# Performance work log

Measured on AMD Instinct MI355X. Metric: run time of the kernel, lower is better.

Reference implementation:

```python
import jax, jax.numpy as jnp
import numpy as np

B, K, D, H, A = 8192, 10, 64, 128, 16
E = K * (K - 1)
# lexicographic ordered pairs (i,j), i != j -- matches adj.nonzero() and sorted(Dict.keys())
_PAIRS = np.array([(i, j) for i in range(K) for j in range(K) if i != j], dtype=np.int32)
SRC = jnp.asarray(_PAIRS[:, 0])  # message for edge (i,j) is aggregated at node i (row)
DST = jnp.asarray(_PAIRS[:, 1])


def setup_inputs() -> dict:
    key = jax.random.key(0)
    k1, k2, k3, k4, k5, k6 = jax.random.split(key, 6)
    F = D + H + A  # node MLP input dim
    return {
        "states": jax.random.normal(k1, (B, K, D), jnp.float32),
        "action_vec": jax.random.normal(k2, (B, K, A), jnp.float32),
        # one Linear(2D -> H) per ordered pair, stacked [E, 2D, H]
        "W_edge": jax.random.normal(k3, (E, 2 * D, H), jnp.float32) * (1.0 / np.sqrt(2 * D)),
        "b_edge": jax.random.normal(k4, (E, H), jnp.float32) * 0.01,
        # one Linear(D+H+A -> D) per node, stacked [K, F, D]
        "W_node": jax.random.normal(k5, (K, F, D), jnp.float32) * (1.0 / np.sqrt(F)),
        "b_node": jax.random.normal(k6, (K, D), jnp.float32) * 0.01,
    }


def reference(states, action_vec, W_edge, b_edge, W_node, b_node):
    # states: [B,K,D], action_vec: [B,K,A]
    b, k, d = states.shape
    # gather endpoints per ordered edge: [B,E,2D]
    pair_feat = jnp.concatenate([states[:, SRC, :], states[:, DST, :]], axis=-1)
    # per-edge-type Linear + tanh, batched as one grouped GEMM: [B,E,H]
    msg = jnp.tanh(jnp.einsum('bef,efh->beh', pair_feat, W_edge) + b_edge)
    # unsorted_segment_sum over source node index (row): [B,K,H]
    agg = jnp.zeros((b, k, msg.shape[-1]), msg.dtype).at[:, SRC, :].add(msg)
    # node input: [x, action, agg] -> per-node Linear + tanh: [B,K,D]
    node_in = jnp.concatenate([states, action_vec, agg], axis=-1)
    out = jnp.tanh(jnp.einsum('bkf,kfd->bkd', node_in, W_node) + b_node)
    return out
```

## Files before the change

kernel.cpp:

```cpp
#include <hip/hip_runtime.h>

typedef _Float16 f16;
typedef _Float16 f16x4 __attribute__((ext_vector_type(4)));
typedef _Float16 f16x8 __attribute__((ext_vector_type(8)));
typedef float    f32x4 __attribute__((ext_vector_type(4)));

#define S2C 2.88539008177792681472f

#define OFF_STF  0u
#define OFF_AC   5242880u
#define OFF_WEF  6553600u
#define OFF_WNF  8028160u
#define OFF_BE2  8171520u
#define OFF_Z    8195840u

__device__ __forceinline__ float fast_exp2(float x){
#if __has_builtin(__builtin_amdgcn_exp2f)
    return __builtin_amdgcn_exp2f(x);
#else
    return exp2f(x);
#endif
}
__device__ __forceinline__ float fast_rcp(float x){
#if __has_builtin(__builtin_amdgcn_rcpf)
    return __builtin_amdgcn_rcpf(x);
#else
    return 1.0f/x;
#endif
}

#define MFMA16(a,b,c) __builtin_amdgcn_mfma_f32_16x16x32_f16(a,b,c,0,0,0)

__global__ void prep(const float* __restrict__ st, const float* __restrict__ ac,
                     const float* __restrict__ We, const float* __restrict__ be,
                     const float* __restrict__ Wn, const float* __restrict__ bn,
                     f16* __restrict__ ws16){
    __shared__ alignas(16) f16 sT[32*132 + 8];
    const int bid = blockIdx.x, t = threadIdx.x;
    if (bid < 2560){
        int g = bid*256 + t;
        int lane = g&63, ks = (g>>6)&1, rt = (g>>7)&1, rg2 = (g>>8)&255, node = g>>16;
        int row = rg2*32 + rt*16 + (lane&15);
        int k   = ks*32 + (lane>>4)*8;
        const float* src = st + ((size_t)row*10 + node)*64 + k;
        const float4 v0 = *(const float4*)src;
        const float4 v1 = *(const float4*)(src+4);
        f16x8 h; h[0]=(f16)v0.x; h[1]=(f16)v0.y; h[2]=(f16)v0.z; h[3]=(f16)v0.w;
                 h[4]=(f16)v1.x; h[5]=(f16)v1.y; h[6]=(f16)v1.z; h[7]=(f16)v1.w;
        *(f16x8*)(ws16 + OFF_STF + (size_t)g*8) = h;
    } else if (bid < 3840){
        int g = (bid-2560)*256 + t;
        const float4 v = ((const float4*)ac)[g];
        f16x4 h; h[0]=(f16)v.x; h[1]=(f16)v.y; h[2]=(f16)v.z; h[3]=(f16)v.w;
        *(f16x4*)(ws16 + OFF_AC + (size_t)g*4) = h;
    } else if (bid < 4200){
        const int eks = bid - 3840;
        const int e = eks >> 2, ks = eks & 3;
        {
            const int r = t >> 3, seg = t & 7;
            const float* src = We + (size_t)e*16384 + (ks*32 + r)*128 + seg*16;
            const float4 v0 = *(const float4*)(src);
            const float4 v1 = *(const float4*)(src+4);
            const float4 v2 = *(const float4*)(src+8);
            const float4 v3 = *(const float4*)(src+12);
            f16x4 h0, h1, h2, h3;
            h0[0]=(f16)v0.x; h0[1]=(f16)v0.y; h0[2]=(f16)v0.z; h0[3]=(f16)v0.w;
            h1[0]=(f16)v1.x; h1[1]=(f16)v1.y; h1[2]=(f16)v1.z; h1[3]=(f16)v1.w;
            h2[0]=(f16)v2.x; h2[1]=(f16)v2.y; h2[2]=(f16)v2.z; h2[3]=(f16)v2.w;
            h3[0]=(f16)v3.x; h3[1]=(f16)v3.y; h3[2]=(f16)v3.z; h3[3]=(f16)v3.w;
            f16* dst = sT + r*132 + seg*16;
            *(f16x4*)(dst)    = h0;  *(f16x4*)(dst+4)  = h1;
            *(f16x4*)(dst+8)  = h2;  *(f16x4*)(dst+12) = h3;
        }
        __syncthreads();
        #pragma unroll
        for (int hh=0; hh<2; ++hh){
            const int gl = t + hh*256;
            const int cg = gl >> 6, lane = gl & 63;
            const int l = lane & 15, q = lane >> 4;
            f16x8 o;
            #pragma unroll
            for (int u=0; u<8; ++u) o[u] = sT[(q*8+u)*132 + cg*16 + l];
            *(f16x8*)(ws16 + OFF_WEF + ((size_t)e*2048 + ks*512 + gl)*8) = o;
        }
    } else if (bid < 4270){
        int g = (bid-4200)*256 + t;
        if (g < 17920){
            int l = g&15, q=(g>>4)&3, c=(g>>6)&3, r=g>>8;
            int ks2 = r % 7, kn = r / 7;
            f16x8 h;
            #pragma unroll
            for (int u=0;u<8;u++){
                int knew = ks2*32 + q*8 + u;
                int f = (knew < 128) ? (knew + 80) : (knew - 128);
                h[u] = (knew < 208) ? (f16)Wn[kn*13312 + f*64 + c*16 + l] : (f16)0.0f;
            }
            *(f16x8*)(ws16 + OFF_WNF + (size_t)kn*14336 + ((size_t)(ks2*4+c)*64 + q*16 + l)*8) = h;
        }
    } else {
        int g = (bid-4270)*256 + t;
        float* be2 = (float*)(ws16 + OFF_BE2);
        if (g < 11520)      be2[g] = S2C*be[g];
        else if (g < 12160) be2[g] = S2C*bn[g-11520];
        else if (g < 12168) ws16[OFF_Z + (g-12160)] = (f16)0.0f;
    }
}

__launch_bounds__(128, 2)
__global__ void gnn_main(const f16* __restrict__ ws16, float* __restrict__ out){
    __shared__ alignas(16) f16 sAgg[32*128];

    const f16* stf = ws16 + OFF_STF;
    const f16* Wef = ws16 + OFF_WEF;
    const float* be2 = (const float*)(ws16 + OFF_BE2);
    const float* bn2 = be2 + 11520;

    const int t = threadIdx.x, lane = t&63, wid = t>>6;
    const int l15 = lane&15, q = lane>>4, qo = q<<3;
    const int i  = blockIdx.x >> 8;
    const int rb = blockIdx.x & 255;
    const int b0 = rb*32;
    const int cs = wid;
    const int e0 = 9*i;

    f16x8 ajb[2][4];
    f16x8 bfb[2][4][4];

    {
        const int j0 = (i==0) ? 1 : 0;
        const f16* p = stf + (size_t)(j0*256 + rb)*2048 + lane*8;
        #pragma unroll
        for (int r=0; r<4; ++r) ajb[0][r] = *(const f16x8*)(p + r*512);
        const f16* wb = Wef + (size_t)(e0*32 + cs*4)*512 + lane*8;
        #pragma unroll
        for (int ks4=0; ks4<4; ++ks4)
            #pragma unroll
            for (int c=0; c<4; ++c)
                bfb[0][ks4][c] = *(const f16x8*)(wb + (ks4*8 + c)*512);
    }
    f16x8 ai[4];
    {
        const f16* p = stf + (size_t)(i*256 + rb)*2048 + lane*8;
        ai[0] = *(const f16x8*)p;        ai[1] = *(const f16x8*)(p+512);
        ai[2] = *(const f16x8*)(p+1024); ai[3] = *(const f16x8*)(p+1536);
    }

    f32x4 agg[2][4] = {};

    #pragma unroll
    for (int e=0; e<9; ++e){
        const int cur = e&1, nxt = cur^1;
        const int ebase = e0 + e;

        if (e < 8){
            const int j2 = (e+1) + ((e+1) >= i);
            const f16* p = stf + (size_t)(j2*256 + rb)*2048 + lane*8;
            #pragma unroll
            for (int r=0; r<4; ++r) ajb[nxt][r] = *(const f16x8*)(p + r*512);
            const f16* wb = Wef + (size_t)((ebase+1)*32 + cs*4)*512 + lane*8;
            #pragma unroll
            for (int ks4=0; ks4<4; ++ks4)
                #pragma unroll
                for (int c=0; c<4; ++c)
                    bfb[nxt][ks4][c] = *(const f16x8*)(wb + (ks4*8 + c)*512);
        }
        float bv[4];
        #pragma unroll
        for (int c=0; c<4; ++c) bv[c] = be2[ebase*128 + cs*64 + c*16 + l15];

        #pragma unroll
        for (int rt=0; rt<2; ++rt){
            f32x4 msg[4] = {};
            #pragma unroll
            for (int ks4=0; ks4<4; ++ks4){
                f16x8 a = (ks4 < 2) ? ai[rt*2 + ks4] : ajb[cur][rt*2 + (ks4-2)];
                #pragma unroll
                for (int c=0; c<4; ++c)
                    msg[c] = MFMA16(a, bfb[cur][ks4][c], msg[c]);
            }
            #pragma unroll
            for (int c=0; c<4; ++c)
                #pragma unroll
                for (int r2=0; r2<4; ++r2){
                    float tt = __builtin_fmaf(msg[c][r2], S2C, bv[c]);
                    float rr = fast_rcp(fast_exp2(tt) + 1.0f);
                    agg[rt][c][r2] = __builtin_fmaf(-2.0f, rr, agg[rt][c][r2]);
                }
        }
    }

    #pragma unroll
    for (int rt=0; rt<2; ++rt)
        #pragma unroll
        for (int c=0; c<4; ++c)
            #pragma unroll
            for (int r2=0; r2<4; ++r2){
                int lrow = rt*16 + q*4 + r2;
                int col  = cs*64 + c*16 + l15;
                sAgg[lrow*128 + (((col>>3) ^ (lrow&7))<<3) + (col&7)] = (f16)(agg[rt][c][r2] + 9.0f);
            }
    __syncthreads();

    f32x4 acc[4] = {};
    const f16* wnb = ws16 + OFF_WNF + (size_t)i*14336;
    const f16* acp = ws16 + OFF_AC;
    const f16* zb  = ws16 + OFF_Z;
    #pragma unroll
    for (int ks2=0; ks2<7; ++ks2){
        f16x8 a;
        if (ks2 < 4){
            int lrow = wid*16 + l15;
            a = *(const f16x8*)(sAgg + lrow*128 + (((ks2*4 + q) ^ (l15&7))<<3));
        } else if (ks2 < 6){
            a = *(const f16x8*)(stf + (size_t)(i*256 + rb)*2048 + wid*1024 + (ks2-4)*512 + lane*8);
        } else {
            int row = b0 + wid*16 + l15;
            const f16* ap = (q < 2) ? (acp + ((size_t)row*10 + i)*16 + qo) : zb;
            a = *(const f16x8*)ap;
        }
        f16x8 bf[4];
        #pragma unroll
        for (int c=0; c<4; ++c)
            bf[c] = *(const f16x8*)(wnb + (size_t)(ks2*4+c)*512 + lane*8);
        #pragma unroll
        for (int c=0; c<4; ++c)
            acc[c] = MFMA16(a, bf[c], acc[c]);
    }
    float bnv[4];
    #pragma unroll
    for (int c=0; c<4; ++c) bnv[c] = bn2[i*64 + c*16 + l15];
    #pragma unroll
    for (int c=0; c<4; ++c)
        #pragma unroll
        for (int r2=0; r2<4; ++r2){
            int row = b0 + wid*16 + q*4 + r2;
            int col = c*16 + l15;
            float tt = __builtin_fmaf(acc[c][r2], S2C, bnv[c]);
            float rr = fast_rcp(fast_exp2(tt) + 1.0f);
            out[((size_t)row*10 + i)*64 + col] = __builtin_fmaf(-2.0f, rr, 1.0f);
        }
}

extern "C" void kernel_launch(void* const* d_in, const int* in_sizes, int n_in,
                              void* d_out, int out_size, void* d_ws, size_t ws_size,
                              hipStream_t stream) {
    const float* states = (const float*)d_in[0];
    const float* action = (const float*)d_in[1];
    const float* W_edge = (const float*)d_in[2];
    const float* b_edge = (const float*)d_in[3];
    const float* W_node = (const float*)d_in[4];
    const float* b_node = (const float*)d_in[5];
    f16* ws16 = (f16*)d_ws;

    hipLaunchKernelGGL(prep, dim3(4318), dim3(256), 0, stream,
                       states, action, W_edge, b_edge, W_node, b_node, ws16);
    hipLaunchKernelGGL(gnn_main, dim3(2560), dim3(128), 0, stream,
                       ws16, (float*)d_out);
}
```

Before: 139.5 us.

## Enlarge blocks to 512 threads, swizzle block order, pair tanh reciprocals

Each block now covers 128 batch rows for one node with 8 waves (4 row groups × 2 column halves) instead of 32 rows with 2 waves, and the grid shrinks to 640 blocks. A swizzled block index spreads nodes across XCDs/CUs. The tanh epilogues now share one reciprocal between two elements (clamped at 60 to avoid overflow), cutting transcendental instruction count. Larger blocks raise LDS use and register pressure under launch_bounds(512,2), and the wid mapping in the node phase must stay consistent with the new row-group layout.

```diff
diff --git a/kernel.cpp b/kernel.cpp
--- a/kernel.cpp
+++ b/kernel.cpp
@@ -106,9 +106,9 @@
     }
 }
 
-__launch_bounds__(128, 2)
+__launch_bounds__(512, 2)
 __global__ void gnn_main(const f16* __restrict__ ws16, float* __restrict__ out){
-    __shared__ alignas(16) f16 sAgg[32*128];
+    __shared__ alignas(16) f16 sAgg[128*128];
 
     const f16* stf = ws16 + OFF_STF;
     const f16* Wef = ws16 + OFF_WEF;
@@ -117,11 +117,14 @@
 
     const int t = threadIdx.x, lane = t&63, wid = t>>6;
     const int l15 = lane&15, q = lane>>4, qo = q<<3;
-    const int i  = blockIdx.x >> 8;
-    const int rb = blockIdx.x & 255;
-    const int b0 = rb*32;
-    const int cs = wid;
+    const int rg = wid>>1, cs = wid&1;
+
+    const int swz = (blockIdx.x & 7)*80 + (blockIdx.x >> 3);
+    const int rb128 = swz / 10;
+    const int i     = swz - rb128*10;
     const int e0 = 9*i;
+    const int rb = rb128*4 + rg;
+    const int b0 = rb128*128;
 
     f16x8 ajb[2][4];
     f16x8 bfb[2][4][4];
@@ -181,10 +184,14 @@
             #pragma unroll
             for (int c=0; c<4; ++c)
                 #pragma unroll
-                for (int r2=0; r2<4; ++r2){
-                    float tt = __builtin_fmaf(msg[c][r2], S2C, bv[c]);
-                    float rr = fast_rcp(fast_exp2(tt) + 1.0f);
-                    agg[rt][c][r2] = __builtin_fmaf(-2.0f, rr, agg[rt][c][r2]);
+                for (int r2=0; r2<4; r2+=2){
+                    float t0 = __builtin_fminf(__builtin_fmaf(msg[c][r2],   S2C, bv[c]), 60.0f);
+                    float t1 = __builtin_fminf(__builtin_fmaf(msg[c][r2+1], S2C, bv[c]), 60.0f);
+                    float a0 = fast_exp2(t0) + 1.0f;
+                    float a1 = fast_exp2(t1) + 1.0f;
+                    float r  = fast_rcp(a0*a1);
+                    agg[rt][c][r2]   = __builtin_fmaf(-2.0f*a1, r, agg[rt][c][r2]);
+                    agg[rt][c][r2+1] = __builtin_fmaf(-2.0f*a0, r, agg[rt][c][r2+1]);
                 }
         }
     }
@@ -195,7 +202,7 @@
         for (int c=0; c<4; ++c)
             #pragma unroll
             for (int r2=0; r2<4; ++r2){
-                int lrow = rt*16 + q*4 + r2;
+                int lrow = rg*32 + rt*16 + q*4 + r2;
                 int col  = cs*64 + c*16 + l15;
                 sAgg[lrow*128 + (((col>>3) ^ (lrow&7))<<3) + (col&7)] = (f16)(agg[rt][c][r2] + 9.0f);
             }
@@ -212,7 +219,8 @@
             int lrow = wid*16 + l15;
             a = *(const f16x8*)(sAgg + lrow*128 + (((ks2*4 + q) ^ (l15&7))<<3));
         } else if (ks2 < 6){
-            a = *(const f16x8*)(stf + (size_t)(i*256 + rb)*2048 + wid*1024 + (ks2-4)*512 + lane*8);
+            a = *(const f16x8*)(stf + (size_t)(i*256 + rb128*4 + (wid>>1))*2048
+                                + (wid&1)*1024 + (ks2-4)*512 + lane*8);
         } else {
             int row = b0 + wid*16 + l15;
             const f16* ap = (q < 2) ? (acp + ((size_t)row*10 + i)*16 + qo) : zb;
@@ -232,12 +240,16 @@
     #pragma unroll
     for (int c=0; c<4; ++c)
         #pragma unroll
-        for (int r2=0; r2<4; ++r2){
-            int row = b0 + wid*16 + q*4 + r2;
-            int col = c*16 + l15;
-            float tt = __builtin_fmaf(acc[c][r2], S2C, bnv[c]);
-            float rr = fast_rcp(fast_exp2(tt) + 1.0f);
-            out[((size_t)row*10 + i)*64 + col] = __builtin_fmaf(-2.0f, rr, 1.0f);
+        for (int r2=0; r2<4; r2+=2){
+            float t0 = __builtin_fminf(__builtin_fmaf(acc[c][r2],   S2C, bnv[c]), 60.0f);
+            float t1 = __builtin_fminf(__builtin_fmaf(acc[c][r2+1], S2C, bnv[c]), 60.0f);
+            float a0 = fast_exp2(t0) + 1.0f;
+            float a1 = fast_exp2(t1) + 1.0f;
+            float r  = fast_rcp(a0*a1);
+            int row0 = b0 + wid*16 + q*4 + r2;
+            int col  = c*16 + l15;
+            out[((size_t)row0*10 + i)*64 + col]     = __builtin_fmaf(-2.0f*a1, r, 1.0f);
+            out[((size_t)(row0+1)*10 + i)*64 + col] = __builtin_fmaf(-2.0f*a0, r, 1.0f);
         }
 }
 
@@ -254,6 +266,6 @@
 
     hipLaunchKernelGGL(prep, dim3(4318), dim3(256), 0, stream,
                        states, action, W_edge, b_edge, W_node, b_node, ws16);
-    hipLaunchKernelGGL(gnn_main, dim3(2560), dim3(128), 0, stream,
+    hipLaunchKernelGGL(gnn_main, dim3(640), dim3(512), 0, stream,
                        ws16, (float*)d_out);
 }
```

New measurement: 147.2 us. +5.5%, slower.
